# Optimization experiments

Hardware: AMD Instinct MI355X
Metric: run time of the kernel (lower is better)

The kernel has to match this reference:

```python
import jax, jax.numpy as jnp
import numpy as np
import math

B, S, D = 4, 2048, 1024
H, HD = 16, 64
RANK = 16
SCALING = 32.0 / RANK  # alpha / rank = 2.0


def setup_inputs() -> dict:
    key = jax.random.key(0)
    ks = jax.random.split(key, 12)
    s = 1.0 / math.sqrt(D)
    inp = {
        "hidden_states": jax.random.normal(ks[0], (B, S, D), dtype=jnp.float32),
        "attention_mask": jnp.zeros((B, 1, 1, S), dtype=jnp.float32),
        "Wq": jax.random.normal(ks[1], (D, D), dtype=jnp.float32) * s,
        "bq": jnp.zeros((D,), dtype=jnp.float32),
        "Aq": jax.random.normal(ks[2], (RANK, D), dtype=jnp.float32) * s,
        "Bq": jax.random.normal(ks[3], (D, RANK), dtype=jnp.float32) * 0.02,
        "Wk": jax.random.normal(ks[4], (D, D), dtype=jnp.float32) * s,
        "bk": jnp.zeros((D,), dtype=jnp.float32),
        "Wv": jax.random.normal(ks[5], (D, D), dtype=jnp.float32) * s,
        "bv": jnp.zeros((D,), dtype=jnp.float32),
        "Av": jax.random.normal(ks[6], (RANK, D), dtype=jnp.float32) * s,
        "Bv": jax.random.normal(ks[7], (D, RANK), dtype=jnp.float32) * 0.02,
        "Wo": jax.random.normal(ks[8], (D, D), dtype=jnp.float32) * s,
        "bo": jnp.zeros((D,), dtype=jnp.float32),
    }
    return inp


def _lora_linear(x, W, b, A, Bm):
    # F.linear(x, W, b) + (x @ A.T @ B.T) * scaling
    return x @ W.T + b + ((x @ A.T) @ Bm.T) * SCALING


def reference(hidden_states, attention_mask, Wq, bq, Aq, Bq, Wk, bk, Wv, bv, Av, Bv, Wo, bo):
    x = hidden_states
    q = _lora_linear(x, Wq, bq, Aq, Bq)          # [B,S,D]
    k = x @ Wk.T + bk                             # [B,S,D]
    v = _lora_linear(x, Wv, bv, Av, Bv)           # [B,S,D]

    def split_heads(t):
        return t.reshape(B, S, H, HD).transpose(0, 2, 1, 3)  # [B,H,S,HD]

    q, k, v = split_heads(q), split_heads(k), split_heads(v)
    scores = jnp.einsum("bhqd,bhkd->bhqk", q, k) / math.sqrt(HD)  # [B,H,S,S]
    scores = scores + attention_mask
    attn = jax.nn.softmax(scores, axis=-1)
    ctx = jnp.einsum("bhqk,bhkd->bhqd", attn, v)  # [B,H,S,HD]
    ctx = ctx.transpose(0, 2, 1, 3).reshape(B, S, D)
    return ctx @ Wo.T + bo
```

## Files before the change

### kernel.cpp

```cpp
#include <hip/hip_runtime.h>
#include <cstdint>


#define D_DIM 1024
#define S_DIM 2048
#define B_DIM 4
#define H_DIM 16
#define HD_DIM 64
#define M_DIM 8192
#define LOG2E 1.44269504f

typedef __bf16 bf16;
typedef __bf16 bf16x4v __attribute__((ext_vector_type(4)));
typedef __bf16 bf16x8 __attribute__((ext_vector_type(8)));
typedef float f32x4 __attribute__((ext_vector_type(4)));
typedef float f32x16 __attribute__((ext_vector_type(16)));

typedef __attribute__((address_space(1))) void* as1p;
typedef __attribute__((address_space(3))) void* as3p;

__device__ __forceinline__ void gll16(const void* g, void* l) {
  __builtin_amdgcn_global_load_lds((as1p)(g), (as3p)(l), 16, 0, 0);
}

__device__ __forceinline__ unsigned pack_bf16x2(float a, float b) {
  union { __bf16 h[2]; unsigned u; } u_;
  u_.h[0] = (bf16)a; u_.h[1] = (bf16)b;
  return u_.u;
}

__device__ __forceinline__ void plswap32(unsigned& a, unsigned& b) {
  asm("v_permlane32_swap_b32 %0, %1" : "+v"(a), "+v"(b));
}

__global__ void convert_x_kernel(const float* __restrict__ x, bf16* __restrict__ xb) {
  const int i = (blockIdx.x * 256 + threadIdx.x) * 8;
  const float4 a = *(const float4*)(x + i);
  const float4 b = *(const float4*)(x + i + 4);
  bf16x8 o;
  o[0] = (bf16)a.x; o[1] = (bf16)a.y; o[2] = (bf16)a.z; o[3] = (bf16)a.w;
  o[4] = (bf16)b.x; o[5] = (bf16)b.y; o[6] = (bf16)b.z; o[7] = (bf16)b.w;
  *(bf16x8*)(xb + i) = o;
}

__global__ void prep_w4_kernel(const float* __restrict__ Wq, const float* __restrict__ Aq,
                               const float* __restrict__ Bq, const float* __restrict__ Wk,
                               const float* __restrict__ Wv, const float* __restrict__ Av,
                               const float* __restrict__ Bv, const float* __restrict__ Wo,
                               bf16* __restrict__ wqkv, bf16* __restrict__ wo) {
  const int sel = blockIdx.y;
  const float* W = (sel == 0) ? Wq : (sel == 1) ? Wk : (sel == 2) ? Wv : Wo;
  const float* A = (sel == 0) ? Aq : (sel == 2) ? Av : nullptr;
  const float* Bm = (sel == 0) ? Bq : (sel == 2) ? Bv : nullptr;
  bf16* out = (sel == 3) ? wo : wqkv + (size_t)sel * D_DIM * D_DIM;
  const int i = blockIdx.x * 256 + threadIdx.x;
  const int n = i >> 10, k = i & (D_DIM - 1);
  float w = W[i];
  if (A) {
    float acc = 0.f;
#pragma unroll
    for (int r = 0; r < 16; ++r) acc = fmaf(Bm[n * 16 + r], A[r * D_DIM + k], acc);
    w += 2.0f * acc;
  }
  out[i] = (bf16)w;
}

__global__ __launch_bounds__(256) void gemm_qkv_kernel(
    const bf16* __restrict__ X, const bf16* __restrict__ Wqkv,
    const float* __restrict__ bq, const float* __restrict__ bk,
    const float* __restrict__ bv, bf16* __restrict__ Qo, bf16* __restrict__ Ko,
    bf16* __restrict__ Vo) {
  __shared__ __attribute__((aligned(16))) bf16 As[2][128 * 64];
  __shared__ __attribute__((aligned(16))) bf16 Bs[2][128 * 64];
  const int tid = threadIdx.x;
  const int wave = tid >> 6, lane = tid & 63;
  const int quad = lane >> 4, l16 = lane & 15;
  const int m0 = blockIdx.x * 128, n0 = blockIdx.y * 128;
  const int wm = (wave >> 1) * 64, wn = (wave & 1) * 64;
  const int srow = lane >> 3, sblk = lane & 7;

  const f32x4 zero = {0.f, 0.f, 0.f, 0.f};
  f32x4 acc[4][4];
#pragma unroll
  for (int mi = 0; mi < 4; ++mi)
#pragma unroll
    for (int ni = 0; ni < 4; ++ni) acc[mi][ni] = zero;

  auto stage = [&](int kt) {
    const int buf = kt & 1, kb = kt * 64;
#pragma unroll
    for (int it = 0; it < 4; ++it) {
      const int c = it * 4 + wave;
      const int row = c * 8 + srow;
      const int b = sblk ^ (row & 7);
      gll16(X + (size_t)(m0 + row) * D_DIM + kb + b * 8, &As[buf][c * 512 + lane * 8]);
      gll16(Wqkv + (size_t)(n0 + row) * D_DIM + kb + b * 8, &Bs[buf][c * 512 + lane * 8]);
    }
  };
  stage(0);

  for (int kt = 0; kt < D_DIM / 64; ++kt) {
    __syncthreads();
    if (kt + 1 < D_DIM / 64) stage(kt + 1);
    const bf16* as_ = &As[kt & 1][0];
    const bf16* bs_ = &Bs[kt & 1][0];
#pragma unroll
    for (int ks = 0; ks < 2; ++ks) {
      bf16x8 af[4], bfr[4];
#pragma unroll
      for (int mi = 0; mi < 4; ++mi) {
        const int row = wm + mi * 16 + l16;
        af[mi] = *(const bf16x8*)(as_ + row * 64 + (((ks * 4 + quad) ^ (row & 7)) * 8));
      }
#pragma unroll
      for (int ni = 0; ni < 4; ++ni) {
        const int row = wn + ni * 16 + l16;
        bfr[ni] = *(const bf16x8*)(bs_ + row * 64 + (((ks * 4 + quad) ^ (row & 7)) * 8));
      }
#pragma unroll
      for (int mi = 0; mi < 4; ++mi)
#pragma unroll
        for (int ni = 0; ni < 4; ++ni)
          acc[mi][ni] =
              __builtin_amdgcn_mfma_f32_16x16x32_bf16(af[mi], bfr[ni], acc[mi][ni], 0, 0, 0);
    }
  }

  const int sel = n0 >> 10;
  const float* bp = (sel == 0) ? bq : (sel == 1) ? bk : bv;
  const float qs = 0.125f * LOG2E;

  if (sel == 2) {
#pragma unroll
    for (int ni = 0; ni < 4; ++ni) {
      const int c = (n0 + wn + ni * 16 + l16) & 1023;
      const int h = c >> 6, hd = c & 63;
      const float bvv = bp[c];
#pragma unroll
      for (int mi = 0; mi < 4; ++mi) {
        const int row0 = m0 + wm + mi * 16 + quad * 4;
        const int b = row0 >> 11, s0 = row0 & (S_DIM - 1);
        bf16x4v pk;
#pragma unroll
        for (int r = 0; r < 4; ++r) pk[r] = (bf16)(acc[mi][ni][r] + bvv);
        *(bf16x4v*)(Vo + ((size_t)(b * H_DIM + h) * HD_DIM + hd) * S_DIM + s0) = pk;
      }
    }
  } else {
    bf16* O = (sel == 0) ? Qo : Ko;
#pragma unroll
    for (int ni = 0; ni < 4; ++ni) {
      const int c = (n0 + wn + ni * 16 + l16) & 1023;
      const int h = c >> 6, hd = c & 63;
      const float bvv = bp[c];
#pragma unroll
      for (int mi = 0; mi < 4; ++mi) {
#pragma unroll
        for (int r = 0; r < 4; ++r) {
          const int row = m0 + wm + mi * 16 + quad * 4 + r;
          const int b = row >> 11, s = row & (S_DIM - 1);
          float v = acc[mi][ni][r] + bvv;
          if (sel == 0) v *= qs;
          O[((size_t)(b * H_DIM + h) * S_DIM + s) * HD_DIM + hd] = (bf16)v;
        }
      }
    }
  }
}

__global__ __launch_bounds__(256) void gemm_o_kernel(const bf16* __restrict__ X,
                                                     const bf16* __restrict__ W,
                                                     const float* __restrict__ bias,
                                                     float* __restrict__ out) {
  __shared__ __attribute__((aligned(16))) bf16 As[2][128 * 64];
  __shared__ __attribute__((aligned(16))) bf16 Bs[2][128 * 64];
  const int tid = threadIdx.x;
  const int wave = tid >> 6, lane = tid & 63;
  const int quad = lane >> 4, l16 = lane & 15;
  const int m0 = blockIdx.x * 128, n0 = blockIdx.y * 128;
  const int wm = (wave >> 1) * 64, wn = (wave & 1) * 64;
  const int srow = lane >> 3, sblk = lane & 7;

  const f32x4 zero = {0.f, 0.f, 0.f, 0.f};
  f32x4 acc[4][4];
#pragma unroll
  for (int mi = 0; mi < 4; ++mi)
#pragma unroll
    for (int ni = 0; ni < 4; ++ni) acc[mi][ni] = zero;

  auto stage = [&](int kt) {
    const int buf = kt & 1, kb = kt * 64;
#pragma unroll
    for (int it = 0; it < 4; ++it) {
      const int c = it * 4 + wave;
      const int row = c * 8 + srow;
      const int b = sblk ^ (row & 7);
      gll16(X + (size_t)(m0 + row) * D_DIM + kb + b * 8, &As[buf][c * 512 + lane * 8]);
      gll16(W + (size_t)(n0 + row) * D_DIM + kb + b * 8, &Bs[buf][c * 512 + lane * 8]);
    }
  };
  stage(0);

  for (int kt = 0; kt < D_DIM / 64; ++kt) {
    __syncthreads();
    if (kt + 1 < D_DIM / 64) stage(kt + 1);
    const bf16* as_ = &As[kt & 1][0];
    const bf16* bs_ = &Bs[kt & 1][0];
#pragma unroll
    for (int ks = 0; ks < 2; ++ks) {
      bf16x8 af[4], bfr[4];
#pragma unroll
      for (int mi = 0; mi < 4; ++mi) {
        const int row = wm + mi * 16 + l16;
        af[mi] = *(const bf16x8*)(as_ + row * 64 + (((ks * 4 + quad) ^ (row & 7)) * 8));
      }
#pragma unroll
      for (int ni = 0; ni < 4; ++ni) {
        const int row = wn + ni * 16 + l16;
        bfr[ni] = *(const bf16x8*)(bs_ + row * 64 + (((ks * 4 + quad) ^ (row & 7)) * 8));
      }
#pragma unroll
      for (int mi = 0; mi < 4; ++mi)
#pragma unroll
        for (int ni = 0; ni < 4; ++ni)
          acc[mi][ni] =
              __builtin_amdgcn_mfma_f32_16x16x32_bf16(af[mi], bfr[ni], acc[mi][ni], 0, 0, 0);
    }
  }
#pragma unroll
  for (int ni = 0; ni < 4; ++ni) {
    const int col = n0 + wn + ni * 16 + l16;
    const float bv = bias[col];
#pragma unroll
    for (int mi = 0; mi < 4; ++mi)
#pragma unroll
      for (int r = 0; r < 4; ++r) {
        const int row = m0 + wm + mi * 16 + quad * 4 + r;
        out[(size_t)row * D_DIM + col] = acc[mi][ni][r] + bv;
      }
  }
}

__global__ __launch_bounds__(256, 4) void attn_kernel(const bf16* __restrict__ Q,
                                                      const bf16* __restrict__ K,
                                                      const bf16* __restrict__ Vt,
                                                      const float* __restrict__ mask,
                                                      bf16* __restrict__ ctx) {
  __shared__ __attribute__((aligned(16))) bf16 Ks[2][32 * 64];
  __shared__ __attribute__((aligned(16))) bf16 Vs[2][64 * 32];
  __shared__ __attribute__((aligned(16))) float cms[S_DIM];

  const int tid = threadIdx.x;
  const int wave = tid >> 6, lane = tid & 63;
  const int l32 = lane & 31, hh = lane >> 5;
  const int bh = blockIdx.y, b = bh >> 4, head = bh & 15;
  const int q0 = blockIdx.x * 128 + wave * 32;

  const bf16* Qg = Q + ((size_t)bh * S_DIM + q0 + l32) * HD_DIM;
  bf16x8 qf[4];
#pragma unroll
  for (int ks = 0; ks < 4; ++ks) qf[ks] = *(const bf16x8*)(Qg + ks * 16 + hh * 8);

  {
    const float* mp = mask + b * S_DIM + tid * 8;
    const float4 a = *(const float4*)(mp);
    const float4 c = *(const float4*)(mp + 4);
    f32x4 r0 = {fmaf(a.x, LOG2E, -16.f), fmaf(a.y, LOG2E, -16.f),
                fmaf(a.z, LOG2E, -16.f), fmaf(a.w, LOG2E, -16.f)};
    f32x4 r1 = {fmaf(c.x, LOG2E, -16.f), fmaf(c.y, LOG2E, -16.f),
                fmaf(c.z, LOG2E, -16.f), fmaf(c.w, LOG2E, -16.f)};
    *(f32x4*)(cms + tid * 8) = r0;
    *(f32x4*)(cms + tid * 8 + 4) = r1;
  }

  bf16x8 onef;
#pragma unroll
  for (int j = 0; j < 8; ++j) onef[j] = (bf16)1.0f;

  f32x16 o[2], osum;
#pragma unroll
  for (int r = 0; r < 16; ++r) { o[0][r] = 0.f; o[1][r] = 0.f; osum[r] = 0.f; }

  const bf16* Kg0 = K + (size_t)bh * S_DIM * HD_DIM;
  const bf16* Vg0 = Vt + (size_t)bh * HD_DIM * S_DIM;

  auto stage = [&](int t) {
    const int buf = t & 1;
    {
      const int row = tid >> 3;
      const int blk = (tid & 7) ^ (row & 7);
      gll16(Kg0 + (size_t)(t * 32 + row) * HD_DIM + blk * 8, &Ks[buf][tid * 8]);
    }
    {
      const int row = tid >> 2;
      const int blk = (tid & 3) ^ ((row >> 1) & 3);
      gll16(Vg0 + (size_t)row * S_DIM + t * 32 + blk * 8, &Vs[buf][tid * 8]);
    }
  };
  stage(0);

  for (int t = 0; t < S_DIM / 32; ++t) {
    __syncthreads();
    if (t + 1 < S_DIM / 32) stage(t + 1);
    const bf16* ks_ = &Ks[t & 1][0];
    const bf16* vs_ = &Vs[t & 1][0];

    f32x16 sc;
    {
      const float* cmb = cms + t * 32 + 4 * hh;
      const f32x4 c0 = *(const f32x4*)(cmb);
      const f32x4 c1 = *(const f32x4*)(cmb + 8);
      const f32x4 c2 = *(const f32x4*)(cmb + 16);
      const f32x4 c3 = *(const f32x4*)(cmb + 24);
#pragma unroll
      for (int r = 0; r < 4; ++r) {
        sc[r] = c0[r]; sc[4 + r] = c1[r]; sc[8 + r] = c2[r]; sc[12 + r] = c3[r];
      }
    }

#pragma unroll
    for (int ks = 0; ks < 4; ++ks) {
      const int blk = ((ks * 2 + hh) ^ (l32 & 7));
      const bf16x8 kf = *(const bf16x8*)(ks_ + l32 * 64 + blk * 8);
      sc = __builtin_amdgcn_mfma_f32_32x32x16_bf16(kf, qf[ks], sc, 0, 0, 0);
    }

    unsigned p[8];
#pragma unroll
    for (int j = 0; j < 8; ++j)
      p[j] = pack_bf16x2(exp2f(sc[2 * j]), exp2f(sc[2 * j + 1]));
    plswap32(p[0], p[2]);
    plswap32(p[1], p[3]);
    plswap32(p[4], p[6]);
    plswap32(p[5], p[7]);
    union { unsigned u[4]; bf16x8 v; } pa0, pa1;
    pa0.u[0] = p[0]; pa0.u[1] = p[1]; pa0.u[2] = p[2]; pa0.u[3] = p[3];
    pa1.u[0] = p[4]; pa1.u[1] = p[5]; pa1.u[2] = p[6]; pa1.u[3] = p[7];

#pragma unroll
    for (int ks = 0; ks < 2; ++ks) {
      const bf16x8 pa = ks ? pa1.v : pa0.v;
#pragma unroll
      for (int nh = 0; nh < 2; ++nh) {
        const int row = nh * 32 + l32;
        const int blk = ((ks * 2 + hh) ^ ((row >> 1) & 3));
        const bf16x8 vf = *(const bf16x8*)(vs_ + row * 32 + blk * 8);
        o[nh] = __builtin_amdgcn_mfma_f32_32x32x16_bf16(pa, vf, o[nh], 0, 0, 0);
      }
      osum = __builtin_amdgcn_mfma_f32_32x32x16_bf16(pa, onef, osum, 0, 0, 0);
    }
  }

#pragma unroll
  for (int r = 0; r < 16; ++r) {
    const float inv = 1.0f / osum[r];
    const int s = q0 + (r & 3) + 8 * (r >> 2) + 4 * hh;
    bf16* cp = ctx + ((size_t)b * S_DIM + s) * D_DIM + head * 64 + l32;
    cp[0] = (bf16)(o[0][r] * inv);
    cp[32] = (bf16)(o[1][r] * inv);
  }
}

extern "C" void kernel_launch(void* const* d_in, const int* in_sizes, int n_in,
                              void* d_out, int out_size, void* d_ws, size_t ws_size,
                              hipStream_t stream) {
  const float* x    = (const float*)d_in[0];
  const float* mask = (const float*)d_in[1];
  const float* Wq   = (const float*)d_in[2];
  const float* bq   = (const float*)d_in[3];
  const float* Aq   = (const float*)d_in[4];
  const float* Bq   = (const float*)d_in[5];
  const float* Wk   = (const float*)d_in[6];
  const float* bk   = (const float*)d_in[7];
  const float* Wv   = (const float*)d_in[8];
  const float* bv   = (const float*)d_in[9];
  const float* Av   = (const float*)d_in[10];
  const float* Bv   = (const float*)d_in[11];
  const float* Wo   = (const float*)d_in[12];
  const float* bo   = (const float*)d_in[13];
  float* out = (float*)d_out;

  bf16* xb   = (bf16*)d_ws;
  bf16* wqkv = xb + (size_t)M_DIM * D_DIM;
  bf16* wo   = wqkv + (size_t)3 * D_DIM * D_DIM;
  bf16* Qw   = wo + (size_t)D_DIM * D_DIM;
  bf16* Kw   = Qw + (size_t)M_DIM * D_DIM;
  bf16* Vw   = Kw + (size_t)M_DIM * D_DIM;
  bf16* Cw   = xb;

  convert_x_kernel<<<M_DIM * D_DIM / (256 * 8), 256, 0, stream>>>(x, xb);
  prep_w4_kernel<<<dim3(D_DIM * D_DIM / 256, 4), 256, 0, stream>>>(
      Wq, Aq, Bq, Wk, Wv, Av, Bv, Wo, wqkv, wo);

  gemm_qkv_kernel<<<dim3(M_DIM / 128, 3 * D_DIM / 128), 256, 0, stream>>>(
      xb, wqkv, bq, bk, bv, Qw, Kw, Vw);

  attn_kernel<<<dim3(S_DIM / 128, B_DIM * H_DIM), 256, 0, stream>>>(Qw, Kw, Vw, mask, Cw);

  gemm_o_kernel<<<dim3(M_DIM / 128, D_DIM / 128), 256, 0, stream>>>(Cw, wo, bo, out);
}
```

Baseline: 345.5 us.

## Process two 32-row query tiles per wave in attention to reuse K/V fragments

Each attention wave now handles 64 query rows (two 32-row sub-tiles) instead of 32, so each block covers 256 queries and the grid halves. K and V fragments read from LDS are reused across both sub-tiles, which halves LDS traffic and global K/V staging per query. In exchange, register pressure roughly doubles for the accumulators (launch bounds relaxed from 4 to 2 blocks per CU), and with only 512 blocks there is less parallelism and occupancy on the GPU.

```diff
diff --git a/kernel.cpp b/kernel.cpp
--- a/kernel.cpp
+++ b/kernel.cpp
@@ -241,7 +241,7 @@
   }
 }
 
-__global__ __launch_bounds__(256, 4) void attn_kernel(const bf16* __restrict__ Q,
+__global__ __launch_bounds__(256, 2) void attn_kernel(const bf16* __restrict__ Q,
                                                       const bf16* __restrict__ K,
                                                       const bf16* __restrict__ Vt,
                                                       const float* __restrict__ mask,
@@ -254,12 +254,15 @@
   const int wave = tid >> 6, lane = tid & 63;
   const int l32 = lane & 31, hh = lane >> 5;
   const int bh = blockIdx.y, b = bh >> 4, head = bh & 15;
-  const int q0 = blockIdx.x * 128 + wave * 32;
-
-  const bf16* Qg = Q + ((size_t)bh * S_DIM + q0 + l32) * HD_DIM;
-  bf16x8 qf[4];
-#pragma unroll
-  for (int ks = 0; ks < 4; ++ks) qf[ks] = *(const bf16x8*)(Qg + ks * 16 + hh * 8);
+  const int q0 = blockIdx.x * 256 + wave * 64;
+
+  const bf16* Qg = Q + ((size_t)bh * S_DIM + q0) * HD_DIM;
+  bf16x8 qf[2][4];
+#pragma unroll
+  for (int qs = 0; qs < 2; ++qs)
+#pragma unroll
+    for (int ks = 0; ks < 4; ++ks)
+      qf[qs][ks] = *(const bf16x8*)(Qg + (qs * 32 + l32) * HD_DIM + ks * 16 + hh * 8);
 
   {
     const float* mp = mask + b * S_DIM + tid * 8;
@@ -277,9 +280,11 @@
 #pragma unroll
   for (int j = 0; j < 8; ++j) onef[j] = (bf16)1.0f;
 
-  f32x16 o[2], osum;
-#pragma unroll
-  for (int r = 0; r < 16; ++r) { o[0][r] = 0.f; o[1][r] = 0.f; osum[r] = 0.f; }
+  f32x16 o[2][2], osum[2];
+#pragma unroll
+  for (int qs = 0; qs < 2; ++qs)
+#pragma unroll
+    for (int r = 0; r < 16; ++r) { o[qs][0][r] = 0.f; o[qs][1][r] = 0.f; osum[qs][r] = 0.f; }
 
   const bf16* Kg0 = K + (size_t)bh * S_DIM * HD_DIM;
   const bf16* Vg0 = Vt + (size_t)bh * HD_DIM * S_DIM;
@@ -305,7 +310,7 @@
     const bf16* ks_ = &Ks[t & 1][0];
     const bf16* vs_ = &Vs[t & 1][0];
 
-    f32x16 sc;
+    f32x16 sc0, sc1;
     {
       const float* cmb = cms + t * 32 + 4 * hh;
       const f32x4 c0 = *(const f32x4*)(cmb);
@@ -314,7 +319,8 @@
       const f32x4 c3 = *(const f32x4*)(cmb + 24);
 #pragma unroll
       for (int r = 0; r < 4; ++r) {
-        sc[r] = c0[r]; sc[4 + r] = c1[r]; sc[8 + r] = c2[r]; sc[12 + r] = c3[r];
+        sc0[r] = c0[r]; sc0[4 + r] = c1[r]; sc0[8 + r] = c2[r]; sc0[12 + r] = c3[r];
+        sc1[r] = c0[r]; sc1[4 + r] = c1[r]; sc1[8 + r] = c2[r]; sc1[12 + r] = c3[r];
       }
     }
 
@@ -322,43 +328,54 @@
     for (int ks = 0; ks < 4; ++ks) {
       const int blk = ((ks * 2 + hh) ^ (l32 & 7));
       const bf16x8 kf = *(const bf16x8*)(ks_ + l32 * 64 + blk * 8);
-      sc = __builtin_amdgcn_mfma_f32_32x32x16_bf16(kf, qf[ks], sc, 0, 0, 0);
-    }
-
-    unsigned p[8];
-#pragma unroll
-    for (int j = 0; j < 8; ++j)
-      p[j] = pack_bf16x2(exp2f(sc[2 * j]), exp2f(sc[2 * j + 1]));
-    plswap32(p[0], p[2]);
-    plswap32(p[1], p[3]);
-    plswap32(p[4], p[6]);
-    plswap32(p[5], p[7]);
-    union { unsigned u[4]; bf16x8 v; } pa0, pa1;
-    pa0.u[0] = p[0]; pa0.u[1] = p[1]; pa0.u[2] = p[2]; pa0.u[3] = p[3];
-    pa1.u[0] = p[4]; pa1.u[1] = p[5]; pa1.u[2] = p[6]; pa1.u[3] = p[7];
-
-#pragma unroll
-    for (int ks = 0; ks < 2; ++ks) {
-      const bf16x8 pa = ks ? pa1.v : pa0.v;
+      sc0 = __builtin_amdgcn_mfma_f32_32x32x16_bf16(kf, qf[0][ks], sc0, 0, 0, 0);
+      sc1 = __builtin_amdgcn_mfma_f32_32x32x16_bf16(kf, qf[1][ks], sc1, 0, 0, 0);
+    }
+
+    bf16x8 vf[2][2];
+#pragma unroll
+    for (int ks = 0; ks < 2; ++ks)
 #pragma unroll
       for (int nh = 0; nh < 2; ++nh) {
         const int row = nh * 32 + l32;
         const int blk = ((ks * 2 + hh) ^ ((row >> 1) & 3));
-        const bf16x8 vf = *(const bf16x8*)(vs_ + row * 32 + blk * 8);
-        o[nh] = __builtin_amdgcn_mfma_f32_32x32x16_bf16(pa, vf, o[nh], 0, 0, 0);
-      }
-      osum = __builtin_amdgcn_mfma_f32_32x32x16_bf16(pa, onef, osum, 0, 0, 0);
-    }
-  }
-
-#pragma unroll
-  for (int r = 0; r < 16; ++r) {
-    const float inv = 1.0f / osum[r];
-    const int s = q0 + (r & 3) + 8 * (r >> 2) + 4 * hh;
-    bf16* cp = ctx + ((size_t)b * S_DIM + s) * D_DIM + head * 64 + l32;
-    cp[0] = (bf16)(o[0][r] * inv);
-    cp[32] = (bf16)(o[1][r] * inv);
-  }
+        vf[nh][ks] = *(const bf16x8*)(vs_ + row * 32 + blk * 8);
+      }
+
+#pragma unroll
+    for (int qs = 0; qs < 2; ++qs) {
+      const f32x16 sc = qs ? sc1 : sc0;
+      unsigned p[8];
+#pragma unroll
+      for (int j = 0; j < 8; ++j)
+        p[j] = pack_bf16x2(exp2f(sc[2 * j]), exp2f(sc[2 * j + 1]));
+      plswap32(p[0], p[2]);
+      plswap32(p[1], p[3]);
+      plswap32(p[4], p[6]);
+      plswap32(p[5], p[7]);
+      union { unsigned u[4]; bf16x8 v; } pa0, pa1;
+      pa0.u[0] = p[0]; pa0.u[1] = p[1]; pa0.u[2] = p[2]; pa0.u[3] = p[3];
+      pa1.u[0] = p[4]; pa1.u[1] = p[5]; pa1.u[2] = p[6]; pa1.u[3] = p[7];
+#pragma unroll
+      for (int ks = 0; ks < 2; ++ks) {
+        const bf16x8 pa = ks ? pa1.v : pa0.v;
+        o[qs][0] = __builtin_amdgcn_mfma_f32_32x32x16_bf16(pa, vf[0][ks], o[qs][0], 0, 0, 0);
+        o[qs][1] = __builtin_amdgcn_mfma_f32_32x32x16_bf16(pa, vf[1][ks], o[qs][1], 0, 0, 0);
+        osum[qs] = __builtin_amdgcn_mfma_f32_32x32x16_bf16(pa, onef, osum[qs], 0, 0, 0);
+      }
+    }
+  }
+
+#pragma unroll
+  for (int qs = 0; qs < 2; ++qs)
+#pragma unroll
+    for (int r = 0; r < 16; ++r) {
+      const float inv = 1.0f / osum[qs][r];
+      const int s = q0 + qs * 32 + (r & 3) + 8 * (r >> 2) + 4 * hh;
+      bf16* cp = ctx + ((size_t)b * S_DIM + s) * D_DIM + head * 64 + l32;
+      cp[0] = (bf16)(o[qs][0][r] * inv);
+      cp[32] = (bf16)(o[qs][1][r] * inv);
+    }
 }
 
 extern "C" void kernel_launch(void* const* d_in, const int* in_sizes, int n_in,
@@ -395,7 +412,7 @@
   gemm_qkv_kernel<<<dim3(M_DIM / 128, 3 * D_DIM / 128), 256, 0, stream>>>(
       xb, wqkv, bq, bk, bv, Qw, Kw, Vw);
 
-  attn_kernel<<<dim3(S_DIM / 128, B_DIM * H_DIM), 256, 0, stream>>>(Qw, Kw, Vw, mask, Cw);
+  attn_kernel<<<dim3(S_DIM / 256, B_DIM * H_DIM), 256, 0, stream>>>(Qw, Kw, Vw, mask, Cw);
 
   gemm_o_kernel<<<dim3(M_DIM / 128, D_DIM / 128), 256, 0, stream>>>(Cw, wo, bo, out);
 }
```

Measured after the change: 337.7 us. 1.02x faster.
